# Kernel optimization log

Hardware: AMD Instinct MI355X
Metric: run time of the kernel (lower is better)

Reference implementation:

```python
import jax, jax.numpy as jnp
import numpy as np

N_NODES = 20000
N_FEAT = 10
EDGE_DIM = 6
D = 256
H = 8
C = D // H  # 32 per-head channels for gat1/gat2
B = 2048
E = 320000
NEG = 0.2        # LeakyReLU slope in GATConv attention
BN_EPS = 1e-5


def _bn_eval(x, g, b):
    # BatchNorm1d in eval mode with fresh buffers: running_mean=0, running_var=1
    return g * x * (1.0 / np.sqrt(1.0 + BN_EPS)) + b


def _gat(x, src, dst, edge_attr, W, a_src, a_dst, We, a_e, bias, heads, out_ch, n):
    # PyG GATConv with edge_dim: shared src/dst linear, per-head additive attention
    xp = (x @ W).reshape(n, heads, out_ch)                       # [N,H,C]
    al_s = jnp.einsum('nhc,hc->nh', xp, a_src)                   # [N,H]
    al_d = jnp.einsum('nhc,hc->nh', xp, a_dst)                   # [N,H]
    ep = (edge_attr @ We).reshape(-1, heads, out_ch)             # [E,H,C]
    al_e = jnp.einsum('ehc,hc->eh', ep, a_e)                     # [E,H]
    alpha = jax.nn.leaky_relu(al_s[src] + al_d[dst] + al_e, NEG)  # [E,H]
    # segment softmax over incoming edges of each dst node
    amax = jax.ops.segment_max(alpha, dst, num_segments=n)
    amax = jnp.where(jnp.isfinite(amax), amax, 0.0)
    ex = jnp.exp(alpha - amax[dst])
    den = jax.ops.segment_sum(ex, dst, num_segments=n)
    w = ex / (den[dst] + 1e-16)
    out = jax.ops.segment_sum(xp[src] * w[..., None], dst, num_segments=n)
    return out.reshape(n, heads * out_ch) + bias


def setup_inputs():
    key = jax.random.key(0)
    ks = iter(jax.random.split(key, 40))
    def rn(shape, scale=0.05):
        return jax.random.normal(next(ks), shape, dtype=jnp.float32) * scale
    inp = {}
    inp['current_node_ids'] = jax.random.randint(next(ks), (B,), 0, N_NODES)
    inp['network_features'] = jax.random.normal(next(ks), (B, N_FEAT), dtype=jnp.float32)
    inp['edge_index'] = jax.random.randint(next(ks), (2, E), 0, N_NODES)
    inp['edge_attr'] = jax.random.normal(next(ks), (E, EDGE_DIM), dtype=jnp.float32)
    inp['emb'] = rn((N_NODES, D), 1.0)
    inp['net_w1'] = rn((N_FEAT, D)); inp['net_b1'] = jnp.zeros((D,), jnp.float32)
    inp['net_g1'] = jnp.ones((D,), jnp.float32); inp['net_be1'] = jnp.zeros((D,), jnp.float32)
    inp['net_w2'] = rn((D, D)); inp['net_b2'] = jnp.zeros((D,), jnp.float32)
    inp['net_g2'] = jnp.ones((D,), jnp.float32); inp['net_be2'] = jnp.zeros((D,), jnp.float32)
    for i, (h, c) in enumerate([(H, C), (H, C), (1, D)], start=1):
        inp[f'gat{i}_W'] = rn((D, h * c))
        inp[f'gat{i}_as'] = rn((h, c)); inp[f'gat{i}_ad'] = rn((h, c))
        inp[f'gat{i}_We'] = rn((EDGE_DIM, h * c)); inp[f'gat{i}_ae'] = rn((h, c))
        inp[f'gat{i}_b'] = jnp.zeros((h * c,), jnp.float32)
    inp['fus_w'] = rn((2 * D, D)); inp['fus_b'] = jnp.zeros((D,), jnp.float32)
    inp['fus_g'] = jnp.ones((D,), jnp.float32); inp['fus_be'] = jnp.zeros((D,), jnp.float32)
    inp['cls_w'] = rn((D, N_NODES)); inp['cls_b'] = jnp.zeros((N_NODES,), jnp.float32)
    return inp


def reference(current_node_ids, network_features, edge_index, edge_attr, emb,
              net_w1, net_b1, net_g1, net_be1, net_w2, net_b2, net_g2, net_be2,
              gat1_W, gat1_as, gat1_ad, gat1_We, gat1_ae, gat1_b,
              gat2_W, gat2_as, gat2_ad, gat2_We, gat2_ae, gat2_b,
              gat3_W, gat3_as, gat3_ad, gat3_We, gat3_ae, gat3_b,
              fus_w, fus_b, fus_g, fus_be, cls_w, cls_b):
    src, dst = edge_index[0], edge_index[1]
    n = emb.shape[0]
    x = jax.nn.relu(_gat(emb, src, dst, edge_attr, gat1_W, gat1_as, gat1_ad, gat1_We, gat1_ae, gat1_b, H, C, n))
    x = jax.nn.relu(_gat(x, src, dst, edge_attr, gat2_W, gat2_as, gat2_ad, gat2_We, gat2_ae, gat2_b, H, C, n))
    x = _gat(x, src, dst, edge_attr, gat3_W, gat3_as, gat3_ad, gat3_We, gat3_ae, gat3_b, 1, D, n)
    node_emb = x[current_node_ids]                               # [B,D]
    h1 = jax.nn.relu(_bn_eval(network_features @ net_w1 + net_b1, net_g1, net_be1))
    net_emb = jax.nn.relu(_bn_eval(h1 @ net_w2 + net_b2, net_g2, net_be2))
    combined = jnp.concatenate([node_emb, net_emb], axis=1)      # [B,2D]
    fused = jax.nn.relu(_bn_eval(combined @ fus_w + fus_b, fus_g, fus_be))
    return fused @ cls_w + cls_b                                 # [B, N_NODES]
```

## Files before the change

### kernel.cpp

```cpp
#include <hip/hip_runtime.h>

#define NEG_SLOPE 0.2f
static constexpr float BN_INV = 0.9999950000374997f;

typedef __bf16 bf16x8 __attribute__((ext_vector_type(8)));
typedef float  f32x4  __attribute__((ext_vector_type(4)));

__device__ inline float4 bf4f(ushort4 u){
  float4 r;
  r.x = __uint_as_float((unsigned)u.x << 16);
  r.y = __uint_as_float((unsigned)u.y << 16);
  r.z = __uint_as_float((unsigned)u.z << 16);
  r.w = __uint_as_float((unsigned)u.w << 16);
  return r;
}
__device__ inline ushort4 f4bf(float4 v){
  ushort4 u;
  u.x = __builtin_bit_cast(unsigned short, (__bf16)v.x);
  u.y = __builtin_bit_cast(unsigned short, (__bf16)v.y);
  u.z = __builtin_bit_cast(unsigned short, (__bf16)v.z);
  u.w = __builtin_bit_cast(unsigned short, (__bf16)v.w);
  return u;
}

__global__ void hist_kernel(const int* __restrict__ dst, int* __restrict__ cnt, int E){
  int e = blockIdx.x*256 + threadIdx.x;
  if (e < E) atomicAdd(&cnt[dst[e]], 1);
}

__global__ __launch_bounds__(1024) void scan1_kernel(int* __restrict__ cnt_cursor,
                                                     int* __restrict__ offs,
                                                     int* __restrict__ bsum, int n){
  __shared__ int wsum[16];
  int tid = threadIdx.x, lane = tid & 63, wv = tid >> 6;
  int i = blockIdx.x*1024 + tid;
  int v = (i < n) ? cnt_cursor[i] : 0;
  int x = v;
#pragma unroll
  for (int off = 1; off < 64; off <<= 1){
    int t = __shfl_up(x, off);
    if (lane >= off) x += t;
  }
  if (lane == 63) wsum[wv] = x;
  __syncthreads();
  int y = (lane < 16) ? wsum[lane] : 0;
#pragma unroll
  for (int off = 1; off < 16; off <<= 1){
    int t = __shfl_up(y, off);
    if (lane >= off) y += t;
  }
  int excl  = (wv == 0) ? 0 : __shfl(y, wv - 1);
  int total = __shfl(y, 15);
  int inc = excl + x;
  if (i < n){ offs[i+1] = inc; cnt_cursor[i] = inc - v; }
  if (tid == 0) bsum[blockIdx.x] = total;
}

__global__ void scan2_kernel(int* __restrict__ bsum, int nb){
  int lane = threadIdx.x;
  int v = (lane < nb) ? bsum[lane] : 0;
  int x = v;
#pragma unroll
  for (int off = 1; off < 64; off <<= 1){
    int t = __shfl_up(x, off);
    if (lane >= off) x += t;
  }
  if (lane < nb) bsum[lane] = x - v;
}

__global__ __launch_bounds__(1024) void scan3_kernel(int* __restrict__ offs, int* __restrict__ cursor,
                                                     const int* __restrict__ bsum, int n){
  int i = blockIdx.x*1024 + threadIdx.x;
  int base = bsum[blockIdx.x];
  if (i < n){ offs[i+1] += base; cursor[i] += base; }
  if (i == 0) offs[0] = 0;
}

__global__ void scatter_kernel(const int* __restrict__ src, const int* __restrict__ dst,
                               const float* __restrict__ ea, int* __restrict__ cursor,
                               int* __restrict__ perm_src, float* __restrict__ ea_perm, int E){
  int e = blockIdx.x*256 + threadIdx.x;
  if (e >= E) return;
  int d = dst[e];
  int pos = atomicAdd(&cursor[d], 1);
  perm_src[pos] = src[e];
#pragma unroll
  for (int k = 0; k < 6; ++k) ea_perm[(size_t)pos*6 + k] = ea[(size_t)e*6 + k];
}

template<bool USE_BIAS, bool USE_BN, bool USE_RELU, typename OutT>
__global__ __launch_bounds__(256) void gemm_kernel(
    const float* __restrict__ A, const float* __restrict__ W,
    const float* __restrict__ bias, const float* __restrict__ gam, const float* __restrict__ bet,
    OutT* __restrict__ C, int M, int N, int K, int LDC)
{
  __shared__ float As[32][68];
  __shared__ float Bs[32][64];
  int tid = threadIdx.x;
  int tx = tid & 15, ty = tid >> 4;
  int bn0 = blockIdx.x * 64, bm0 = blockIdx.y * 64;
  float acc[4][4] = {};
  for (int k0 = 0; k0 < K; k0 += 32){
    int kk = tid & 31, mm0 = tid >> 5;
#pragma unroll
    for (int r = 0; r < 8; ++r){
      int ml = mm0 + r*8;
      int m = bm0 + ml;
      As[kk][ml] = (m < M) ? A[(size_t)m*K + k0 + kk] : 0.f;
    }
    int nn = tid & 63, kb = tid >> 6;
#pragma unroll
    for (int r = 0; r < 8; ++r){
      int kl = kb + r*4;
      int n = bn0 + nn;
      Bs[kl][nn] = (n < N) ? W[(size_t)(k0 + kl)*N + n] : 0.f;
    }
    __syncthreads();
#pragma unroll
    for (int k = 0; k < 32; ++k){
      float4 a4 = *reinterpret_cast<const float4*>(&As[k][ty*4]);
      float4 b4 = *reinterpret_cast<const float4*>(&Bs[k][tx*4]);
      acc[0][0] += a4.x*b4.x; acc[0][1] += a4.x*b4.y; acc[0][2] += a4.x*b4.z; acc[0][3] += a4.x*b4.w;
      acc[1][0] += a4.y*b4.x; acc[1][1] += a4.y*b4.y; acc[1][2] += a4.y*b4.z; acc[1][3] += a4.y*b4.w;
      acc[2][0] += a4.z*b4.x; acc[2][1] += a4.z*b4.y; acc[2][2] += a4.z*b4.z; acc[2][3] += a4.z*b4.w;
      acc[3][0] += a4.w*b4.x; acc[3][1] += a4.w*b4.y; acc[3][2] += a4.w*b4.z; acc[3][3] += a4.w*b4.w;
    }
    __syncthreads();
  }
#pragma unroll
  for (int i = 0; i < 4; ++i){
    int m = bm0 + ty*4 + i;
    if (m < M){
#pragma unroll
      for (int j = 0; j < 4; ++j){
        int n = bn0 + tx*4 + j;
        if (n < N){
          float c = acc[i][j];
          if (USE_BIAS) c += bias[n];
          if (USE_BN)   c = gam[n]*c*BN_INV + bet[n];
          if (USE_RELU) c = fmaxf(c, 0.f);
          C[(size_t)m*LDC + n] = (OutT)c;
        }
      }
    }
  }
}

__global__ void wtrans_kernel(const float* __restrict__ W, __bf16* __restrict__ Wt, int K, int N){
  __shared__ float tile[32][33];
  int n0 = blockIdx.x*32, k0 = blockIdx.y*32;
  int t = threadIdx.x;
  int nl = t & 31, kl = t >> 5;
#pragma unroll
  for (int r = 0; r < 4; ++r)
    tile[kl + r*8][nl] = W[(size_t)(k0 + kl + r*8)*N + n0 + nl];
  __syncthreads();
  int nl2 = t >> 3, kc = (t & 7)*4;
#pragma unroll
  for (int j = 0; j < 4; ++j)
    Wt[(size_t)(n0 + nl2)*K + k0 + kc + j] = (__bf16)tile[kc + j][nl2];
}

__global__ void wtrans3_kernel(const float* __restrict__ W0, const float* __restrict__ W1,
                               const float* __restrict__ W2, __bf16* __restrict__ Wt,
                               const float* __restrict__ We1, const float* __restrict__ ae1,
                               const float* __restrict__ We2, const float* __restrict__ ae2,
                               const float* __restrict__ We3, const float* __restrict__ ae3,
                               float* __restrict__ M){
  if (blockIdx.z == 3){
    if (blockIdx.x != 0 || blockIdx.y != 0) return;
    int t = threadIdx.x;
    if (t < 96){
      const float* We = (t < 48) ? We1 : We2;
      const float* ae = (t < 48) ? ae1 : ae2;
      int u = t % 48, k = u / 8, h = u % 8;
      float s = 0.f;
      for (int c = 0; c < 32; ++c) s += We[k*256 + h*32 + c] * ae[h*32 + c];
      M[t] = s;
    } else if (t < 102){
      int k = t - 96;
      float s = 0.f;
      for (int c = 0; c < 256; ++c) s += We3[k*256 + c] * ae3[c];
      M[t] = s;
    }
    return;
  }
  __shared__ float tile[32][33];
  const float* W = (blockIdx.z == 0) ? W0 : (blockIdx.z == 1) ? W1 : W2;
  __bf16* D = Wt + (size_t)blockIdx.z * 65536;
  int n0 = blockIdx.x*32, k0 = blockIdx.y*32;
  int t = threadIdx.x;
  int nl = t & 31, kl = t >> 5;
#pragma unroll
  for (int r = 0; r < 4; ++r)
    tile[kl + r*8][nl] = W[(size_t)(k0 + kl + r*8)*256 + n0 + nl];
  __syncthreads();
  int nl2 = t >> 3, kc = (t & 7)*4;
#pragma unroll
  for (int j = 0; j < 4; ++j)
    D[(size_t)(n0 + nl2)*256 + k0 + kc + j] = (__bf16)tile[kc + j][nl2];
}

template<bool USE_BIAS, bool AF32, int ALSD, typename OutT>
__global__ __launch_bounds__(256) void mfma_gemm_kernel(
    const void* __restrict__ Aptr, const __bf16* __restrict__ Bt,
    const float* __restrict__ bias, OutT* __restrict__ C, int M, int N, int K,
    const float* __restrict__ a_s, const float* __restrict__ a_d,
    float* __restrict__ als, float* __restrict__ ald)
{
  const __bf16* Ab = (const __bf16*)Aptr;
  const float*  Af = (const float*) Aptr;
  __shared__ __bf16 As[128*72];
  __shared__ __bf16 Bs[128*72];
  int tid = threadIdx.x;
  int lane = tid & 63, w = tid >> 6;
  int quad = lane >> 4, l16 = lane & 15;
  int wm = (w & 1) * 64, wn = (w >> 1) * 64;
  int bn0 = blockIdx.x * 128, bm0 = blockIdx.y * 128;
  f32x4 acc[4][4] = {};
  for (int k0 = 0; k0 < K; k0 += 64){
#pragma unroll
    for (int p = 0; p < 4; ++p){
      int idx = p*256 + tid;
      int row = idx >> 3, ch = idx & 7;
      uint4 av;
      if constexpr (AF32){
        av = make_uint4(0,0,0,0);
        int m = bm0 + row;
        if (m < M){
          const float4* A4 = reinterpret_cast<const float4*>(&Af[(size_t)m*K + k0 + ch*8]);
          float4 x0 = A4[0], x1 = A4[1];
          ushort4 u0 = f4bf(x0), u1 = f4bf(x1);
          av = make_uint4((unsigned)u0.x | ((unsigned)u0.y << 16),
                          (unsigned)u0.z | ((unsigned)u0.w << 16),
                          (unsigned)u1.x | ((unsigned)u1.y << 16),
                          (unsigned)u1.z | ((unsigned)u1.w << 16));
        }
      } else {
        av = *reinterpret_cast<const uint4*>(&Ab[(size_t)(bm0 + row)*K + k0 + ch*8]);
      }
      *reinterpret_cast<uint4*>(&As[row*72 + ch*8]) = av;
      int n = bn0 + row;
      uint4 bv = make_uint4(0,0,0,0);
      if (n < N) bv = *reinterpret_cast<const uint4*>(&Bt[(size_t)n*K + k0 + ch*8]);
      *reinterpret_cast<uint4*>(&Bs[row*72 + ch*8]) = bv;
    }
    __syncthreads();
#pragma unroll
    for (int s = 0; s < 2; ++s){
      bf16x8 af[4], bfr[4];
#pragma unroll
      for (int t4 = 0; t4 < 4; ++t4){
        af[t4]  = *reinterpret_cast<const bf16x8*>(&As[(wm + t4*16 + l16)*72 + s*32 + quad*8]);
        bfr[t4] = *reinterpret_cast<const bf16x8*>(&Bs[(wn + t4*16 + l16)*72 + s*32 + quad*8]);
      }
#pragma unroll
      for (int mt = 0; mt < 4; ++mt)
#pragma unroll
        for (int nt = 0; nt < 4; ++nt)
          acc[mt][nt] = __builtin_amdgcn_mfma_f32_16x16x32_bf16(af[mt], bfr[nt], acc[mt][nt], 0, 0, 0);
    }
    __syncthreads();
  }
#pragma unroll
  for (int mt = 0; mt < 4; ++mt){
#pragma unroll
    for (int nt = 0; nt < 4; ++nt){
      int n = bn0 + wn + nt*16 + l16;
      if (n < N){
        float bv = USE_BIAS ? bias[n] : 0.f;
#pragma unroll
        for (int r = 0; r < 4; ++r){
          int m = bm0 + wm + mt*16 + quad*4 + r;
          if (m < M) C[(size_t)m*N + n] = (OutT)(acc[mt][nt][r] + bv);
        }
      }
    }
  }
  if constexpr (ALSD == 8){
    float av4[4], dv4[4];
#pragma unroll
    for (int nt = 0; nt < 4; ++nt){
      int n = bn0 + wn + nt*16 + l16;
      av4[nt] = a_s[n];
      dv4[nt] = a_d[n];
    }
    int hb = (bn0 + wn) >> 5;
#pragma unroll
    for (int mt = 0; mt < 4; ++mt){
#pragma unroll
      for (int r = 0; r < 4; ++r){
        float s0 = acc[mt][0][r]*av4[0] + acc[mt][1][r]*av4[1];
        float s1 = acc[mt][2][r]*av4[2] + acc[mt][3][r]*av4[3];
        float d0 = acc[mt][0][r]*dv4[0] + acc[mt][1][r]*dv4[1];
        float d1 = acc[mt][2][r]*dv4[2] + acc[mt][3][r]*dv4[3];
#pragma unroll
        for (int off = 1; off < 16; off <<= 1){
          s0 += __shfl_xor(s0, off); s1 += __shfl_xor(s1, off);
          d0 += __shfl_xor(d0, off); d1 += __shfl_xor(d1, off);
        }
        if (l16 == 0){
          int m = bm0 + wm + mt*16 + quad*4 + r;
          if (m < M){
            als[m*8 + hb]     = s0; als[m*8 + hb + 1] = s1;
            ald[m*8 + hb]     = d0; ald[m*8 + hb + 1] = d1;
          }
        }
      }
    }
  }
}

__global__ void alsd1_kernel(const __bf16* __restrict__ xp, const float* __restrict__ a_s,
                             const float* __restrict__ a_d, float* __restrict__ als,
                             float* __restrict__ ald, int Nn){
  int gid = blockIdx.x*blockDim.x + threadIdx.x;
  int wave = gid >> 6, lane = threadIdx.x & 63;
  if (wave >= Nn) return;
  float4 xv = bf4f(reinterpret_cast<const ushort4*>(xp)[(size_t)wave*64 + lane]);
  float4 av = reinterpret_cast<const float4*>(a_s)[lane];
  float4 dv = reinterpret_cast<const float4*>(a_d)[lane];
  float ps = xv.x*av.x + xv.y*av.y + xv.z*av.z + xv.w*av.w;
  float pd = xv.x*dv.x + xv.y*dv.y + xv.z*dv.z + xv.w*dv.w;
#pragma unroll
  for (int off = 1; off < 64; off <<= 1){ ps += __shfl_xor(ps,off); pd += __shfl_xor(pd,off); }
  if (lane == 0){ als[wave] = ps; ald[wave] = pd; }
}

__global__ void agg8_kernel(const int* __restrict__ offs, const int* __restrict__ perm_src,
                            const float* __restrict__ ea_perm, const float* __restrict__ Mf,
                            const float* __restrict__ als, const float* __restrict__ ald,
                            const __bf16* __restrict__ xp, const float* __restrict__ bias,
                            __bf16* __restrict__ out, int Nn){
  int gid = blockIdx.x*blockDim.x + threadIdx.x;
  int wave = gid >> 6, lane = threadIdx.x & 63;
  if (wave >= Nn) return;
  int beg = offs[wave], end = offs[wave+1];
  int hsel = lane >> 3;

  float mk[6];
#pragma unroll
  for (int k = 0; k < 6; ++k) mk[k] = Mf[k*8 + hsel];
  float aldv = ald[(size_t)wave*8 + hsel];

  const ushort4* X4 = reinterpret_cast<const ushort4*>(xp);
  float4 acc = make_float4(0.f,0.f,0.f,0.f);
  float den = 0.f;

  int i = beg;
  for (; i + 3 < end; i += 4){
    int s0 = perm_src[i], s1 = perm_src[i+1], s2 = perm_src[i+2], s3 = perm_src[i+3];
    float a0 = als[(size_t)s0*8 + hsel] + aldv;
    float a1 = als[(size_t)s1*8 + hsel] + aldv;
    float a2 = als[(size_t)s2*8 + hsel] + aldv;
    float a3 = als[(size_t)s3*8 + hsel] + aldv;
#pragma unroll
    for (int k = 0; k < 6; ++k){
      a0 += ea_perm[(size_t)i*6 + k]     * mk[k];
      a1 += ea_perm[(size_t)(i+1)*6 + k] * mk[k];
      a2 += ea_perm[(size_t)(i+2)*6 + k] * mk[k];
      a3 += ea_perm[(size_t)(i+3)*6 + k] * mk[k];
    }
    a0 = (a0 > 0.f) ? a0 : NEG_SLOPE*a0;
    a1 = (a1 > 0.f) ? a1 : NEG_SLOPE*a1;
    a2 = (a2 > 0.f) ? a2 : NEG_SLOPE*a2;
    a3 = (a3 > 0.f) ? a3 : NEG_SLOPE*a3;
    float e0 = __expf(a0), e1 = __expf(a1), e2 = __expf(a2), e3 = __expf(a3);
    den += (e0 + e1) + (e2 + e3);
    float4 x0 = bf4f(X4[(size_t)s0*64 + lane]);
    float4 x1 = bf4f(X4[(size_t)s1*64 + lane]);
    float4 x2 = bf4f(X4[(size_t)s2*64 + lane]);
    float4 x3 = bf4f(X4[(size_t)s3*64 + lane]);
    acc.x += x0.x*e0 + x1.x*e1 + x2.x*e2 + x3.x*e3;
    acc.y += x0.y*e0 + x1.y*e1 + x2.y*e2 + x3.y*e3;
    acc.z += x0.z*e0 + x1.z*e1 + x2.z*e2 + x3.z*e3;
    acc.w += x0.w*e0 + x1.w*e1 + x2.w*e2 + x3.w*e3;
  }
  for (; i < end; ++i){
    int s = perm_src[i];
    float a = als[(size_t)s*8 + hsel] + aldv;
#pragma unroll
    for (int k = 0; k < 6; ++k) a += ea_perm[(size_t)i*6 + k] * mk[k];
    a = (a > 0.f) ? a : NEG_SLOPE*a;
    float e = __expf(a);
    den += e;
    float4 xv = bf4f(X4[(size_t)s*64 + lane]);
    acc.x += xv.x*e; acc.y += xv.y*e; acc.z += xv.z*e; acc.w += xv.w*e;
  }

  float r = 1.f / (den + 1e-16f);
  float4 bv = reinterpret_cast<const float4*>(bias)[lane];
  acc.x = fmaxf(acc.x*r + bv.x, 0.f); acc.y = fmaxf(acc.y*r + bv.y, 0.f);
  acc.z = fmaxf(acc.z*r + bv.z, 0.f); acc.w = fmaxf(acc.w*r + bv.w, 0.f);
  reinterpret_cast<ushort4*>(out)[(size_t)wave*64 + lane] = f4bf(acc);
}

__global__ void agg1q_kernel(const int* __restrict__ ids, const int* __restrict__ offs,
                             const int* __restrict__ perm_src, const float* __restrict__ ea_perm,
                             const float* __restrict__ Mf, const float* __restrict__ als,
                             const float* __restrict__ ald, const __bf16* __restrict__ xp,
                             const float* __restrict__ bias, float* __restrict__ comb, int B){
  int gid = blockIdx.x*blockDim.x + threadIdx.x;
  int wave = gid >> 6, lane = threadIdx.x & 63;
  if (wave >= B) return;
  int node = ids[wave];
  int beg = offs[node], end = offs[node+1];

  float mk[6];
#pragma unroll
  for (int k = 0; k < 6; ++k) mk[k] = Mf[k];
  float aldv = ald[node];

  const ushort4* X4 = reinterpret_cast<const ushort4*>(xp);
  float4 acc = make_float4(0.f,0.f,0.f,0.f);
  float den = 0.f;

  int i = beg;
  for (; i + 3 < end; i += 4){
    int s0 = perm_src[i], s1 = perm_src[i+1], s2 = perm_src[i+2], s3 = perm_src[i+3];
    float a0 = als[s0] + aldv, a1 = als[s1] + aldv;
    float a2 = als[s2] + aldv, a3 = als[s3] + aldv;
#pragma unroll
    for (int k = 0; k < 6; ++k){
      a0 += ea_perm[(size_t)i*6 + k]     * mk[k];
      a1 += ea_perm[(size_t)(i+1)*6 + k] * mk[k];
      a2 += ea_perm[(size_t)(i+2)*6 + k] * mk[k];
      a3 += ea_perm[(size_t)(i+3)*6 + k] * mk[k];
    }
    a0 = (a0 > 0.f) ? a0 : NEG_SLOPE*a0;
    a1 = (a1 > 0.f) ? a1 : NEG_SLOPE*a1;
    a2 = (a2 > 0.f) ? a2 : NEG_SLOPE*a2;
    a3 = (a3 > 0.f) ? a3 : NEG_SLOPE*a3;
    float e0 = __expf(a0), e1 = __expf(a1), e2 = __expf(a2), e3 = __expf(a3);
    den += (e0 + e1) + (e2 + e3);
    float4 x0 = bf4f(X4[(size_t)s0*64 + lane]);
    float4 x1 = bf4f(X4[(size_t)s1*64 + lane]);
    float4 x2 = bf4f(X4[(size_t)s2*64 + lane]);
    float4 x3 = bf4f(X4[(size_t)s3*64 + lane]);
    acc.x += x0.x*e0 + x1.x*e1 + x2.x*e2 + x3.x*e3;
    acc.y += x0.y*e0 + x1.y*e1 + x2.y*e2 + x3.y*e3;
    acc.z += x0.z*e0 + x1.z*e1 + x2.z*e2 + x3.z*e3;
    acc.w += x0.w*e0 + x1.w*e1 + x2.w*e2 + x3.w*e3;
  }
  for (; i < end; ++i){
    int s = perm_src[i];
    float a = als[s] + aldv;
#pragma unroll
    for (int k = 0; k < 6; ++k) a += ea_perm[(size_t)i*6 + k] * mk[k];
    a = (a > 0.f) ? a : NEG_SLOPE*a;
    float e = __expf(a);
    den += e;
    float4 xv = bf4f(X4[(size_t)s*64 + lane]);
    acc.x += xv.x*e; acc.y += xv.y*e; acc.z += xv.z*e; acc.w += xv.w*e;
  }

  float r = 1.f / (den + 1e-16f);
  float4 bv = reinterpret_cast<const float4*>(bias)[lane];
  acc.x = acc.x*r + bv.x; acc.y = acc.y*r + bv.y;
  acc.z = acc.z*r + bv.z; acc.w = acc.w*r + bv.w;
  reinterpret_cast<float4*>(comb)[(size_t)wave*128 + lane] = acc;
}

__global__ void h1_kernel(const float* __restrict__ nf, const float* __restrict__ w1,
                          const float* __restrict__ b1, const float* __restrict__ g,
                          const float* __restrict__ be, float* __restrict__ out){
  int b = blockIdx.x, j = threadIdx.x;
  float s = b1[j];
#pragma unroll
  for (int k = 0; k < 10; ++k) s += nf[b*10 + k] * w1[k*256 + j];
  s = g[j]*s*BN_INV + be[j];
  out[b*256 + j] = fmaxf(s, 0.f);
}

extern "C" void kernel_launch(void* const* d_in, const int* in_sizes, int n_in,
                              void* d_out, int out_size, void* d_ws, size_t ws_size,
                              hipStream_t stream)
{
  const int*   ids   = (const int*)  d_in[0];
  const float* nf    = (const float*)d_in[1];
  const int*   eidx  = (const int*)  d_in[2];
  const float* eattr = (const float*)d_in[3];
  const float* emb   = (const float*)d_in[4];
  const float* w1    = (const float*)d_in[5];
  const float* b1    = (const float*)d_in[6];
  const float* g1    = (const float*)d_in[7];
  const float* be1   = (const float*)d_in[8];
  const float* w2    = (const float*)d_in[9];
  const float* b2    = (const float*)d_in[10];
  const float* g2    = (const float*)d_in[11];
  const float* be2   = (const float*)d_in[12];
  const float* gW[3]  = {(const float*)d_in[13], (const float*)d_in[19], (const float*)d_in[25]};
  const float* gas[3] = {(const float*)d_in[14], (const float*)d_in[20], (const float*)d_in[26]};
  const float* gad[3] = {(const float*)d_in[15], (const float*)d_in[21], (const float*)d_in[27]};
  const float* gWe[3] = {(const float*)d_in[16], (const float*)d_in[22], (const float*)d_in[28]};
  const float* gae[3] = {(const float*)d_in[17], (const float*)d_in[23], (const float*)d_in[29]};
  const float* gb[3]  = {(const float*)d_in[18], (const float*)d_in[24], (const float*)d_in[30]};
  const float* fus_w  = (const float*)d_in[31];
  const float* fus_b  = (const float*)d_in[32];
  const float* fus_g  = (const float*)d_in[33];
  const float* fus_be = (const float*)d_in[34];
  const float* cls_w  = (const float*)d_in[35];
  const float* cls_b  = (const float*)d_in[36];

  const int E  = in_sizes[3] / 6;
  const int Nn = in_sizes[4] / 256;
  const int B  = in_sizes[0];
  const int Ncls = in_sizes[36];
  const int Npad = (Nn + 127) & ~127;
  const int* src = eidx;
  const int* dst = eidx + E;

  char* wbase = (char*)d_ws;
  size_t woff = 0;
  auto carve = [&](size_t bytes)->void*{
    void* p = wbase + woff;
    woff = (woff + bytes + 255) & ~(size_t)255;
    return p;
  };
  int*    offs     = (int*)   carve((size_t)(Nn+1)*4);
  int*    cursor   = (int*)   carve((size_t)Nn*4);
  int*    bsum     = (int*)   carve(64*4);
  int*    perm_src = (int*)   carve((size_t)E*4);
  float*  ea_perm  = (float*) carve((size_t)E*6*4);
  __bf16* xb0      = (__bf16*)carve((size_t)Npad*256*2);
  __bf16* xb1      = (__bf16*)carve((size_t)Npad*256*2);
  __bf16* xpb      = (__bf16*)carve((size_t)Npad*256*2);
  __bf16* gWt      = (__bf16*)carve((size_t)3*256*256*2);
  float*  als      = (float*) carve((size_t)Nn*8*4);
  float*  ald      = (float*) carve((size_t)Nn*8*4);
  float*  Mfold    = (float*) carve(128*4);
  float*  h1b      = (float*) carve((size_t)B*256*4);
  float*  comb     = (float*) carve((size_t)B*512*4);
  __bf16* fusedb   = (__bf16*)carve((size_t)B*256*2);
  __bf16* clsWt    = (__bf16*)carve((size_t)Ncls*256*2);
  (void)ws_size; (void)n_in; (void)out_size;

  const int nb1024 = (Nn + 1023) / 1024;

  hipMemsetAsync(cursor, 0, (size_t)Nn*4, stream);
  hist_kernel<<<(E+255)/256, 256, 0, stream>>>(dst, cursor, E);
  scan1_kernel<<<nb1024, 1024, 0, stream>>>(cursor, offs, bsum, Nn);
  scan2_kernel<<<1, 64, 0, stream>>>(bsum, nb1024);
  scan3_kernel<<<nb1024, 1024, 0, stream>>>(offs, cursor, bsum, Nn);
  scatter_kernel<<<(E+255)/256, 256, 0, stream>>>(src, dst, eattr, cursor,
                                                  perm_src, ea_perm, E);

  wtrans3_kernel<<<dim3(8, 8, 4), 256, 0, stream>>>(gW[0], gW[1], gW[2], gWt,
                                                    gWe[0], gae[0], gWe[1], gae[1],
                                                    gWe[2], gae[2], Mfold);
  wtrans_kernel<<<dim3(Ncls/32, 256/32), 256, 0, stream>>>(cls_w, clsWt, 256, Ncls);

  dim3 mfma_grid_xp(2, Npad/128);
  int node_blocks = (Nn*64 + 255)/256;

  mfma_gemm_kernel<false, true, 8, __bf16><<<mfma_grid_xp, 256, 0, stream>>>(
      emb, gWt, nullptr, xpb, Nn, 256, 256, gas[0], gad[0], als, ald);
  agg8_kernel<<<node_blocks, 256, 0, stream>>>(offs, perm_src, ea_perm, Mfold,
                                               als, ald, xpb, gb[0], xb1, Nn);
  mfma_gemm_kernel<false, false, 8, __bf16><<<mfma_grid_xp, 256, 0, stream>>>(
      xb1, gWt + 65536, nullptr, xpb, Nn, 256, 256, gas[1], gad[1], als, ald);
  agg8_kernel<<<node_blocks, 256, 0, stream>>>(offs, perm_src, ea_perm, Mfold + 48,
                                               als, ald, xpb, gb[1], xb0, Nn);
  mfma_gemm_kernel<false, false, 0, __bf16><<<mfma_grid_xp, 256, 0, stream>>>(
      xb0, gWt + 131072, nullptr, xpb, Nn, 256, 256, nullptr, nullptr, nullptr, nullptr);
  alsd1_kernel<<<node_blocks, 256, 0, stream>>>(xpb, gas[2], gad[2], als, ald, Nn);
  agg1q_kernel<<<(B*64 + 255)/256, 256, 0, stream>>>(ids, offs, perm_src, ea_perm,
                                                     Mfold + 96, als, ald, xpb, gb[2], comb, B);

  h1_kernel<<<B, 256, 0, stream>>>(nf, w1, b1, g1, be1, h1b);
  gemm_kernel<true,true,true,float><<<dim3(4, B/64), 256, 0, stream>>>(
      h1b, w2, b2, g2, be2, comb + 256, B, 256, 256, 512);

  gemm_kernel<true,true,true,__bf16><<<dim3(4, B/64), 256, 0, stream>>>(
      comb, fus_w, fus_b, fus_g, fus_be, fusedb, B, 256, 512, 256);
  mfma_gemm_kernel<true, false, 0, float><<<dim3((Ncls+127)/128, B/128), 256, 0, stream>>>(
      fusedb, clsWt, cls_b, (float*)d_out, B, Ncls, 256, nullptr, nullptr, nullptr, nullptr);
}
```

Measured before the change: 711.3 us.

## Add dedicated 256x128 classifier GEMM and fuse gat3 attention logits into GEMM

Replaces the generic 128x128 MFMA GEMM for the large classifier output with a 512-thread kernel that uses 256x128 tiles and remaps block indices so that consecutive workgroups are spread across the M-tiles of one N-stripe, to improve reuse of the cls weights and reduce launch count. It also folds the single-head attention logit computation for the third GAT layer into the GEMM epilogue via atomicAdd into zeroed buffers. That removes the separate alsd1 pass over xp. The zeroing is merged into the existing memset. Atomics add nondeterministic summation order, and the classifier kernel assumes B is a multiple of 256 and Ncls/128 tile count divisible by 8.

```diff
diff --git a/kernel.cpp b/kernel.cpp
--- a/kernel.cpp
+++ b/kernel.cpp
@@ -201,10 +201,10 @@
     D[(size_t)(n0 + nl2)*256 + k0 + kc + j] = (__bf16)tile[kc + j][nl2];
 }
 
-template<bool USE_BIAS, bool AF32, int ALSD, typename OutT>
+template<bool AF32, int ALSD, typename OutT>
 __global__ __launch_bounds__(256) void mfma_gemm_kernel(
     const void* __restrict__ Aptr, const __bf16* __restrict__ Bt,
-    const float* __restrict__ bias, OutT* __restrict__ C, int M, int N, int K,
+    OutT* __restrict__ C, int M, int N, int K,
     const float* __restrict__ a_s, const float* __restrict__ a_d,
     float* __restrict__ als, float* __restrict__ ald)
 {
@@ -268,16 +268,15 @@
     for (int nt = 0; nt < 4; ++nt){
       int n = bn0 + wn + nt*16 + l16;
       if (n < N){
-        float bv = USE_BIAS ? bias[n] : 0.f;
 #pragma unroll
         for (int r = 0; r < 4; ++r){
           int m = bm0 + wm + mt*16 + quad*4 + r;
-          if (m < M) C[(size_t)m*N + n] = (OutT)(acc[mt][nt][r] + bv);
+          if (m < M) C[(size_t)m*N + n] = (OutT)(acc[mt][nt][r]);
         }
       }
     }
   }
-  if constexpr (ALSD == 8){
+  if constexpr (ALSD != 0){
     float av4[4], dv4[4];
 #pragma unroll
     for (int nt = 0; nt < 4; ++nt){
@@ -302,8 +301,13 @@
         if (l16 == 0){
           int m = bm0 + wm + mt*16 + quad*4 + r;
           if (m < M){
-            als[m*8 + hb]     = s0; als[m*8 + hb + 1] = s1;
-            ald[m*8 + hb]     = d0; ald[m*8 + hb + 1] = d1;
+            if constexpr (ALSD == 8){
+              als[m*8 + hb]     = s0; als[m*8 + hb + 1] = s1;
+              ald[m*8 + hb]     = d0; ald[m*8 + hb + 1] = d1;
+            } else {
+              atomicAdd(&als[m], s0 + s1);
+              atomicAdd(&ald[m], d0 + d1);
+            }
           }
         }
       }
@@ -311,20 +315,70 @@
   }
 }
 
-__global__ void alsd1_kernel(const __bf16* __restrict__ xp, const float* __restrict__ a_s,
-                             const float* __restrict__ a_d, float* __restrict__ als,
-                             float* __restrict__ ald, int Nn){
-  int gid = blockIdx.x*blockDim.x + threadIdx.x;
-  int wave = gid >> 6, lane = threadIdx.x & 63;
-  if (wave >= Nn) return;
-  float4 xv = bf4f(reinterpret_cast<const ushort4*>(xp)[(size_t)wave*64 + lane]);
-  float4 av = reinterpret_cast<const float4*>(a_s)[lane];
-  float4 dv = reinterpret_cast<const float4*>(a_d)[lane];
-  float ps = xv.x*av.x + xv.y*av.y + xv.z*av.z + xv.w*av.w;
-  float pd = xv.x*dv.x + xv.y*dv.y + xv.z*dv.z + xv.w*dv.w;
-#pragma unroll
-  for (int off = 1; off < 64; off <<= 1){ ps += __shfl_xor(ps,off); pd += __shfl_xor(pd,off); }
-  if (lane == 0){ als[wave] = ps; ald[wave] = pd; }
+__global__ __launch_bounds__(512) void mfma_cls_kernel(
+    const __bf16* __restrict__ A, const __bf16* __restrict__ Bt,
+    const float* __restrict__ bias, float* __restrict__ C, int M, int N, int K)
+{
+  __shared__ __bf16 As[256*72];
+  __shared__ __bf16 Bs[128*72];
+  int tid = threadIdx.x;
+  int lane = tid & 63, w = tid >> 6;
+  int quad = lane >> 4, l16 = lane & 15;
+  int wm = (w >> 1) * 64, wn = (w & 1) * 64;
+  int nwg = gridDim.x;
+  int chunk = nwg >> 3;
+  int orig = (blockIdx.x & 7) * chunk + (blockIdx.x >> 3);
+  int bm0 = (orig & 7) * 256, bn0 = (orig >> 3) * 128;
+  f32x4 acc[4][4] = {};
+  for (int k0 = 0; k0 < K; k0 += 64){
+#pragma unroll
+    for (int p = 0; p < 4; ++p){
+      int idx = p*512 + tid;
+      int row = idx >> 3, ch = idx & 7;
+      uint4 av = *reinterpret_cast<const uint4*>(&A[(size_t)(bm0 + row)*K + k0 + ch*8]);
+      *reinterpret_cast<uint4*>(&As[row*72 + ch*8]) = av;
+    }
+#pragma unroll
+    for (int p = 0; p < 2; ++p){
+      int idx = p*512 + tid;
+      int row = idx >> 3, ch = idx & 7;
+      int n = bn0 + row;
+      uint4 bv = make_uint4(0,0,0,0);
+      if (n < N) bv = *reinterpret_cast<const uint4*>(&Bt[(size_t)n*K + k0 + ch*8]);
+      *reinterpret_cast<uint4*>(&Bs[row*72 + ch*8]) = bv;
+    }
+    __syncthreads();
+#pragma unroll
+    for (int s = 0; s < 2; ++s){
+      bf16x8 af[4], bfr[4];
+#pragma unroll
+      for (int t4 = 0; t4 < 4; ++t4){
+        af[t4]  = *reinterpret_cast<const bf16x8*>(&As[(wm + t4*16 + l16)*72 + s*32 + quad*8]);
+        bfr[t4] = *reinterpret_cast<const bf16x8*>(&Bs[(wn + t4*16 + l16)*72 + s*32 + quad*8]);
+      }
+#pragma unroll
+      for (int mt = 0; mt < 4; ++mt)
+#pragma unroll
+        for (int nt = 0; nt < 4; ++nt)
+          acc[mt][nt] = __builtin_amdgcn_mfma_f32_16x16x32_bf16(af[mt], bfr[nt], acc[mt][nt], 0, 0, 0);
+    }
+    __syncthreads();
+  }
+#pragma unroll
+  for (int mt = 0; mt < 4; ++mt){
+#pragma unroll
+    for (int nt = 0; nt < 4; ++nt){
+      int n = bn0 + wn + nt*16 + l16;
+      if (n < N){
+        float bv = bias[n];
+#pragma unroll
+        for (int r = 0; r < 4; ++r){
+          int m = bm0 + wm + mt*16 + quad*4 + r;
+          C[(size_t)m*N + n] = acc[mt][nt][r] + bv;
+        }
+      }
+    }
+  }
 }
 
 __global__ void agg8_kernel(const int* __restrict__ offs, const int* __restrict__ perm_src,
@@ -519,6 +573,9 @@
   };
   int*    offs     = (int*)   carve((size_t)(Nn+1)*4);
   int*    cursor   = (int*)   carve((size_t)Nn*4);
+  float*  als3     = (float*) carve((size_t)Nn*4);
+  float*  ald3     = (float*) carve((size_t)Nn*4);
+  size_t  zero_bytes = (size_t)((char*)ald3 - (char*)cursor) + (size_t)Nn*4;
   int*    bsum     = (int*)   carve(64*4);
   int*    perm_src = (int*)   carve((size_t)E*4);
   float*  ea_perm  = (float*) carve((size_t)E*6*4);
@@ -537,7 +594,7 @@
 
   const int nb1024 = (Nn + 1023) / 1024;
 
-  hipMemsetAsync(cursor, 0, (size_t)Nn*4, stream);
+  hipMemsetAsync(cursor, 0, zero_bytes, stream);
   hist_kernel<<<(E+255)/256, 256, 0, stream>>>(dst, cursor, E);
   scan1_kernel<<<nb1024, 1024, 0, stream>>>(cursor, offs, bsum, Nn);
   scan2_kernel<<<1, 64, 0, stream>>>(bsum, nb1024);
@@ -553,19 +610,18 @@
   dim3 mfma_grid_xp(2, Npad/128);
   int node_blocks = (Nn*64 + 255)/256;
 
-  mfma_gemm_kernel<false, true, 8, __bf16><<<mfma_grid_xp, 256, 0, stream>>>(
-      emb, gWt, nullptr, xpb, Nn, 256, 256, gas[0], gad[0], als, ald);
+  mfma_gemm_kernel<true, 8, __bf16><<<mfma_grid_xp, 256, 0, stream>>>(
+      emb, gWt, xpb, Nn, 256, 256, gas[0], gad[0], als, ald);
   agg8_kernel<<<node_blocks, 256, 0, stream>>>(offs, perm_src, ea_perm, Mfold,
                                                als, ald, xpb, gb[0], xb1, Nn);
-  mfma_gemm_kernel<false, false, 8, __bf16><<<mfma_grid_xp, 256, 0, stream>>>(
-      xb1, gWt + 65536, nullptr, xpb, Nn, 256, 256, gas[1], gad[1], als, ald);
+  mfma_gemm_kernel<false, 8, __bf16><<<mfma_grid_xp, 256, 0, stream>>>(
+      xb1, gWt + 65536, xpb, Nn, 256, 256, gas[1], gad[1], als, ald);
   agg8_kernel<<<node_blocks, 256, 0, stream>>>(offs, perm_src, ea_perm, Mfold + 48,
                                                als, ald, xpb, gb[1], xb0, Nn);
-  mfma_gemm_kernel<false, false, 0, __bf16><<<mfma_grid_xp, 256, 0, stream>>>(
-      xb0, gWt + 131072, nullptr, xpb, Nn, 256, 256, nullptr, nullptr, nullptr, nullptr);
-  alsd1_kernel<<<node_blocks, 256, 0, stream>>>(xpb, gas[2], gad[2], als, ald, Nn);
+  mfma_gemm_kernel<false, 1, __bf16><<<mfma_grid_xp, 256, 0, stream>>>(
+      xb0, gWt + 131072, xpb, Nn, 256, 256, gas[2], gad[2], als3, ald3);
   agg1q_kernel<<<(B*64 + 255)/256, 256, 0, stream>>>(ids, offs, perm_src, ea_perm,
-                                                     Mfold + 96, als, ald, xpb, gb[2], comb, B);
+                                                     Mfold + 96, als3, ald3, xpb, gb[2], comb, B);
 
   h1_kernel<<<B, 256, 0, stream>>>(nf, w1, b1, g1, be1, h1b);
   gemm_kernel<true,true,true,float><<<dim3(4, B/64), 256, 0, stream>>>(
@@ -573,6 +629,7 @@
 
   gemm_kernel<true,true,true,__bf16><<<dim3(4, B/64), 256, 0, stream>>>(
       comb, fus_w, fus_b, fus_g, fus_be, fusedb, B, 256, 512, 256);
-  mfma_gemm_kernel<true, false, 0, float><<<dim3((Ncls+127)/128, B/128), 256, 0, stream>>>(
-      fusedb, clsWt, cls_b, (float*)d_out, B, Ncls, 256, nullptr, nullptr, nullptr, nullptr);
-}
+  const int NB = (Ncls + 127) / 128;
+  mfma_cls_kernel<<<8*NB, 512, 0, stream>>>(fusedb, clsWt, cls_b, (float*)d_out,
+                                            B, Ncls, 256);
+}
```

New measurement: 672.9 us. 1.06x faster.
